# Optimization experiments

Measured on AMD Instinct MI355X. Metric: run time of the kernel, lower is better.

## Reference

```python
import jax, jax.numpy as jnp
import numpy as np
import math

B, S, D = 1024, 64, 512
H, DQ, DK = 8, 64, 64
SCALE = 1.0 / math.sqrt(D)


def setup_inputs() -> dict:
    key = jax.random.key(0)
    k1, k2, k3, k4 = jax.random.split(key, 4)
    query = jax.random.normal(k1, (B, S, D), dtype=jnp.float32)
    context = jax.random.normal(k2, (B, S, D), dtype=jnp.float32)
    # nn.Linear(input_dim, n_head*dq) weights (stored as [out, in] in torch; use [in, out] here)
    Wq = jax.random.normal(k3, (D, H * DQ), dtype=jnp.float32) * (1.0 / math.sqrt(D))
    bq = jnp.zeros((H * DQ,), dtype=jnp.float32)
    Wc = jax.random.normal(k4, (D, H * DK), dtype=jnp.float32) * (1.0 / math.sqrt(D))
    bc = jnp.zeros((H * DK,), dtype=jnp.float32)
    return {"query": query, "context": context, "Wq": Wq, "bq": bq, "Wc": Wc, "bc": bc}


def reference(query, context, Wq, bq, Wc, bc):
    bs, seq_len, _ = query.shape
    # projections -> [B, H, S, d]
    q = (query @ Wq + bq).reshape(bs, seq_len, H, DQ).transpose(0, 2, 1, 3)
    c = (context @ Wc + bc).reshape(bs, seq_len, H, DK).transpose(0, 2, 1, 3)
    # shared score matrix [B, H, Sq, Sk]
    attn = jnp.einsum('bhqd,bhkd->bhqk', q, c) * SCALE
    # direction 1: softmax over keys; NOTE: as written in the torch source,
    # the second bmm operand is the TRANSPOSED c_proj [*, d_k, S], so the
    # contraction pairs attn's key axis with c's FEATURE axis (requires S==d_k).
    c_attn = jax.nn.softmax(attn, axis=-1)
    c_coattn = jnp.einsum('bhqk,bhjk->bhqj', c_attn, c)  # [B,H,S,S(=d_k)]
    # direction 2: softmax over queries, transpose, standard weighted sum of q
    q_attn = jax.nn.softmax(attn, axis=2)
    q_coattn = jnp.einsum('bhqk,bhqd->bhkd', q_attn, q)  # [B,H,S,d_q]
    # [B, H, S, d] -> [B, S, H*d]
    c_out = c_coattn.transpose(0, 2, 1, 3).reshape(bs, seq_len, H * DK)
    q_out = q_coattn.transpose(0, 2, 1, 3).reshape(bs, seq_len, H * DQ)
    return (c_out, q_out)
```

## Files before the change

kernel.cpp:

```cpp
#include <hip/hip_runtime.h>
#include <hip/hip_bf16.h>

typedef float  f32x4 __attribute__((ext_vector_type(4)));
typedef short  s16x8 __attribute__((ext_vector_type(8)));

#define NB   1024
#define SEQ  64
#define DIM  512
#define NH   8
#define SCALE 0.044194173824159216f

static __device__ __forceinline__ unsigned short f2bf(float f) {
    unsigned u = __builtin_bit_cast(unsigned, f);
    return (unsigned short)((u + 0x8000u) >> 16);
}

static __device__ __forceinline__ f32x4 mma(s16x8 a, s16x8 b, f32x4 c) {
    return __builtin_amdgcn_mfma_f32_16x16x32_bf16(a, b, c, 0, 0, 0);
}

static __device__ __forceinline__ s16x8 cvt2(float4 a, float4 b) {
    s16x8 x;
    x[0] = (short)f2bf(a.x); x[1] = (short)f2bf(a.y);
    x[2] = (short)f2bf(a.z); x[3] = (short)f2bf(a.w);
    x[4] = (short)f2bf(b.x); x[5] = (short)f2bf(b.y);
    x[6] = (short)f2bf(b.z); x[7] = (short)f2bf(b.w);
    return x;
}

__global__ __launch_bounds__(256) void prep_weights(
    const float* __restrict__ Wq, const float* __restrict__ Wc,
    unsigned short* __restrict__ wf)
{
    int gid  = blockIdx.x * 256 + threadIdx.x;
    int m    = gid >> 15;
    int tile = (gid >> 10) & 31;
    int ks   = (gid >> 6) & 15;
    int lane = gid & 63;
    const float* W = m ? Wc : Wq;
    int col = tile * 16 + (lane & 15);
    int k0  = ks * 32 + (lane >> 4) * 8;
    unsigned short* dst = wf + (size_t)gid * 8;
#pragma unroll
    for (int j = 0; j < 8; ++j)
        dst[j] = f2bf(W[(size_t)(k0 + j) * DIM + col]);
}

__global__ __launch_bounds__(512) void fused_b(
    const float* __restrict__ query,
    const float* __restrict__ context,
    const float* __restrict__ bq,
    const float* __restrict__ bc,
    const unsigned short* __restrict__ wf,
    float* __restrict__ out)
{
    __shared__ unsigned short smem[69632];
    unsigned short* Q = smem;
    unsigned short* C = smem + 32768;

    const int tid  = threadIdx.x;
    const int lane = tid & 63;
    const int wv   = tid >> 6;
    const int l15  = lane & 15;
    const int l4   = lane >> 4;
    const int b    = blockIdx.x;

    const float* gq = query   + (size_t)b * SEQ * DIM;
    const float* gc = context + (size_t)b * SEQ * DIM;

    {
        const int row = tid >> 3;
        const int cw  = tid & 7;
        const int wsb = (cw >> 2) * 256 + (cw & 3) * 64 + row;
        const float* sq = gq + (size_t)row * DIM + cw * 8;
        const float* sc = gc + (size_t)row * DIM + cw * 8;
        float4 lq[16], lc[16];
#pragma unroll
        for (int p = 0; p < 8; ++p) {
            lq[2 * p]     = *(const float4*)(sq + p * 64);
            lq[2 * p + 1] = *(const float4*)(sq + p * 64 + 4);
        }
#pragma unroll
        for (int p = 0; p < 8; ++p) {
            lc[2 * p]     = *(const float4*)(sc + p * 64);
            lc[2 * p + 1] = *(const float4*)(sc + p * 64 + 4);
        }
#pragma unroll
        for (int p = 0; p < 8; ++p) {
            *(s16x8*)&Q[((p * 512 + wsb) ^ cw) * 8] = cvt2(lq[2 * p], lq[2 * p + 1]);
            *(s16x8*)&C[((p * 512 + wsb) ^ cw) * 8] = cvt2(lc[2 * p], lc[2 * p + 1]);
        }
    }
    __syncthreads();

    const f32x4 fz = {0.f, 0.f, 0.f, 0.f};
    f32x4 acc[4][4];

#pragma unroll
    for (int x = 0; x < 4; ++x)
#pragma unroll
        for (int y = 0; y < 4; ++y) acc[x][y] = fz;

    {
        const unsigned short* wfm = wf + 262144;
#pragma unroll
        for (int ks = 0; ks < 16; ++ks) {
            const int p  = ks >> 1;
            const int kk = ks & 1;
            s16x8 af[4], bf[4];
#pragma unroll
            for (int mt = 0; mt < 4; ++mt) {
                const int s = p * 512 + kk * 256 + l4 * 64 + mt * 16 + l15;
                af[mt] = *(const s16x8*)&C[(s ^ (4 * kk + l4)) * 8];
            }
#pragma unroll
            for (int nt = 0; nt < 4; ++nt)
                bf[nt] = *(const s16x8*)(wfm +
                         ((size_t)((wv * 4 + nt) * 16 + ks) * 64 + lane) * 8);
#pragma unroll
            for (int mt = 0; mt < 4; ++mt)
#pragma unroll
                for (int nt = 0; nt < 4; ++nt)
                    acc[mt][nt] = mma(af[mt], bf[nt], acc[mt][nt]);
        }
    }
    __syncthreads();

    unsigned short (*T)[72] = (unsigned short(*)[72])(C + wv * 4608);

#pragma unroll
    for (int nt = 0; nt < 4; ++nt) {
        float bcv = bc[wv * 64 + nt * 16 + l15];
#pragma unroll
        for (int mt = 0; mt < 4; ++mt)
#pragma unroll
            for (int r = 0; r < 4; ++r)
                T[mt * 16 + l4 * 4 + r][nt * 16 + l15] = f2bf(acc[mt][nt][r] + bcv);
    }
    s16x8 cb[4][2];
#pragma unroll
    for (int nt = 0; nt < 4; ++nt)
#pragma unroll
        for (int ks = 0; ks < 2; ++ks)
            cb[nt][ks] = *(const s16x8*)&T[nt * 16 + l15][ks * 32 + l4 * 8];

#pragma unroll
    for (int x = 0; x < 4; ++x)
#pragma unroll
        for (int y = 0; y < 4; ++y) acc[x][y] = fz;

    {
#pragma unroll
        for (int ks = 0; ks < 16; ++ks) {
            const int p  = ks >> 1;
            const int kk = ks & 1;
            s16x8 af[4], bf[4];
#pragma unroll
            for (int mt = 0; mt < 4; ++mt) {
                const int s = p * 512 + kk * 256 + l4 * 64 + mt * 16 + l15;
                af[mt] = *(const s16x8*)&Q[(s ^ (4 * kk + l4)) * 8];
            }
#pragma unroll
            for (int nt = 0; nt < 4; ++nt)
                bf[nt] = *(const s16x8*)(wf +
                         ((size_t)((wv * 4 + nt) * 16 + ks) * 64 + lane) * 8);
#pragma unroll
            for (int mt = 0; mt < 4; ++mt)
#pragma unroll
                for (int nt = 0; nt < 4; ++nt)
                    acc[mt][nt] = mma(af[mt], bf[nt], acc[mt][nt]);
        }
    }

#pragma unroll
    for (int nt = 0; nt < 4; ++nt) {
        float bqv = bq[wv * 64 + nt * 16 + l15];
#pragma unroll
        for (int mt = 0; mt < 4; ++mt)
#pragma unroll
            for (int r = 0; r < 4; ++r)
                T[mt * 16 + l4 * 4 + r][nt * 16 + l15] = f2bf(acc[mt][nt][r] + bqv);
    }
    s16x8 qa[4][2], qb[4][2];
#pragma unroll
    for (int mt = 0; mt < 4; ++mt)
#pragma unroll
        for (int ks = 0; ks < 2; ++ks)
            qa[mt][ks] = *(const s16x8*)&T[mt * 16 + l15][ks * 32 + l4 * 8];
#pragma unroll
    for (int nt = 0; nt < 4; ++nt)
#pragma unroll
        for (int ks = 0; ks < 2; ++ks) {
            s16x8 v;
#pragma unroll
            for (int j = 0; j < 8; ++j)
                v[j] = (short)T[ks * 32 + l4 * 8 + j][nt * 16 + l15];
            qb[nt][ks] = v;
        }

    f32x4 Sc[4][4];
#pragma unroll
    for (int x = 0; x < 4; ++x)
#pragma unroll
        for (int y = 0; y < 4; ++y) Sc[x][y] = fz;
#pragma unroll
    for (int ks = 0; ks < 2; ++ks)
#pragma unroll
        for (int mt = 0; mt < 4; ++mt)
#pragma unroll
            for (int nt = 0; nt < 4; ++nt)
                Sc[mt][nt] = mma(qa[mt][ks], cb[nt][ks], Sc[mt][nt]);

#pragma unroll
    for (int mt = 0; mt < 4; ++mt)
#pragma unroll
        for (int r = 0; r < 4; ++r) {
            float m = fmaxf(fmaxf(Sc[mt][0][r], Sc[mt][1][r]),
                            fmaxf(Sc[mt][2][r], Sc[mt][3][r]));
            m = fmaxf(m, __shfl_xor(m, 1));
            m = fmaxf(m, __shfl_xor(m, 2));
            m = fmaxf(m, __shfl_xor(m, 4));
            m = fmaxf(m, __shfl_xor(m, 8));
            float e[4], s = 0.f;
#pragma unroll
            for (int nt = 0; nt < 4; ++nt) { e[nt] = __expf(SCALE * (Sc[mt][nt][r] - m)); s += e[nt]; }
            s += __shfl_xor(s, 1);
            s += __shfl_xor(s, 2);
            s += __shfl_xor(s, 4);
            s += __shfl_xor(s, 8);
            float inv = 1.f / s;
            int row = mt * 16 + l4 * 4 + r;
#pragma unroll
            for (int nt = 0; nt < 4; ++nt)
                T[row][nt * 16 + l15] = f2bf(e[nt] * inv);
        }

    s16x8 pa[4][2];
#pragma unroll
    for (int mt = 0; mt < 4; ++mt)
#pragma unroll
        for (int ks = 0; ks < 2; ++ks)
            pa[mt][ks] = *(const s16x8*)&T[mt * 16 + l15][ks * 32 + l4 * 8];

#pragma unroll
    for (int nt = 0; nt < 4; ++nt) {
        float m = -1e30f;
#pragma unroll
        for (int mt = 0; mt < 4; ++mt)
#pragma unroll
            for (int r = 0; r < 4; ++r) m = fmaxf(m, Sc[mt][nt][r]);
        m = fmaxf(m, __shfl_xor(m, 16));
        m = fmaxf(m, __shfl_xor(m, 32));
        float ee[4][4], s = 0.f;
#pragma unroll
        for (int mt = 0; mt < 4; ++mt)
#pragma unroll
            for (int r = 0; r < 4; ++r) { ee[mt][r] = __expf(SCALE * (Sc[mt][nt][r] - m)); s += ee[mt][r]; }
        s += __shfl_xor(s, 16);
        s += __shfl_xor(s, 32);
        float inv = 1.f / s;
        int krow = nt * 16 + l15;
#pragma unroll
        for (int mt = 0; mt < 4; ++mt)
#pragma unroll
            for (int r = 0; r < 4; ++r)
                T[krow][mt * 16 + l4 * 4 + r] = f2bf(ee[mt][r] * inv);
    }

    f32x4 O[4][4];
#pragma unroll
    for (int x = 0; x < 4; ++x)
#pragma unroll
        for (int y = 0; y < 4; ++y) O[x][y] = fz;
#pragma unroll
    for (int ks = 0; ks < 2; ++ks)
#pragma unroll
        for (int mt = 0; mt < 4; ++mt)
#pragma unroll
            for (int nt = 0; nt < 4; ++nt)
                O[mt][nt] = mma(pa[mt][ks], cb[nt][ks], O[mt][nt]);

    float* cO = out;
#pragma unroll
    for (int mt = 0; mt < 4; ++mt)
#pragma unroll
        for (int nt = 0; nt < 4; ++nt)
#pragma unroll
            for (int r = 0; r < 4; ++r) {
                int qrow = mt * 16 + l4 * 4 + r;
                cO[((size_t)b * SEQ + qrow) * (NH * 64) + wv * 64 + nt * 16 + l15] = O[mt][nt][r];
            }

    s16x8 p2a[4][2];
#pragma unroll
    for (int mt = 0; mt < 4; ++mt)
#pragma unroll
        for (int ks = 0; ks < 2; ++ks)
            p2a[mt][ks] = *(const s16x8*)&T[mt * 16 + l15][ks * 32 + l4 * 8];

#pragma unroll
    for (int x = 0; x < 4; ++x)
#pragma unroll
        for (int y = 0; y < 4; ++y) O[x][y] = fz;
#pragma unroll
    for (int ks = 0; ks < 2; ++ks)
#pragma unroll
        for (int mt = 0; mt < 4; ++mt)
#pragma unroll
            for (int nt = 0; nt < 4; ++nt)
                O[mt][nt] = mma(p2a[mt][ks], qb[nt][ks], O[mt][nt]);

    float* qO = out + (size_t)NB * SEQ * NH * 64;
#pragma unroll
    for (int mt = 0; mt < 4; ++mt)
#pragma unroll
        for (int nt = 0; nt < 4; ++nt)
#pragma unroll
            for (int r = 0; r < 4; ++r) {
                int krow = mt * 16 + l4 * 4 + r;
                qO[((size_t)b * SEQ + krow) * (NH * 64) + wv * 64 + nt * 16 + l15] = O[mt][nt][r];
            }
}

extern "C" void kernel_launch(void* const* d_in, const int* in_sizes, int n_in,
                              void* d_out, int out_size, void* d_ws, size_t ws_size,
                              hipStream_t stream) {
    const float* query   = (const float*)d_in[0];
    const float* context = (const float*)d_in[1];
    const float* Wq      = (const float*)d_in[2];
    const float* bq      = (const float*)d_in[3];
    const float* Wc      = (const float*)d_in[4];
    const float* bc      = (const float*)d_in[5];
    float* out = (float*)d_out;

    unsigned short* wfrag = (unsigned short*)d_ws;

    prep_weights<<<256, 256, 0, stream>>>(Wq, Wc, wfrag);
    fused_b<<<NB, 512, 0, stream>>>(query, context, bq, bc, wfrag, out);
}
```

Measured before the change: 181.6 us.

## Pre-swizzle activations to bf16 and stream tiles via global_load_lds in persistent kernel

```diff
diff --git a/kernel.cpp b/kernel.cpp
--- a/kernel.cpp
+++ b/kernel.cpp
@@ -46,6 +46,288 @@
         dst[j] = f2bf(W[(size_t)(k0 + j) * DIM + col]);
 }
 
+__global__ __launch_bounds__(256) void prep_acts_swz(
+    const float* __restrict__ qin, const float* __restrict__ cin,
+    unsigned short* __restrict__ acts)
+{
+    size_t g0 = ((size_t)blockIdx.x * 256 + threadIdx.x) * 2;
+#pragma unroll
+    for (int t = 0; t < 2; ++t) {
+        size_t g  = g0 + t;
+        int    d  = (int)(g & 4095);
+        size_t tb = g >> 12;
+        const float* act = (tb >= NB)
+            ? cin + (tb - NB) * (size_t)SEQ * DIM
+            : qin + tb * (size_t)SEQ * DIM;
+        int p  = d >> 9, kk = (d >> 8) & 1, qq = (d >> 6) & 3;
+        int row = (d & 63) ^ (4 * kk + qq);
+        const float* src = act + (size_t)row * DIM + p * 64 + kk * 32 + qq * 8;
+        float4 a  = *(const float4*)src;
+        float4 b2 = *(const float4*)(src + 4);
+        *(s16x8*)(acts + g * 8) = cvt2(a, b2);
+    }
+}
+
+#define GLL16(GP, LP)                                                          \
+    __builtin_amdgcn_global_load_lds(                                          \
+        (const unsigned int __attribute__((address_space(1)))*)(const void*)(GP), \
+        (unsigned int __attribute__((address_space(3)))*)(void*)(LP), 16, 0, 0)
+
+__global__ __launch_bounds__(512) void fused_gll(
+    const unsigned short* __restrict__ acts,
+    const float* __restrict__ bq,
+    const float* __restrict__ bc,
+    const unsigned short* __restrict__ wf,
+    float* __restrict__ out)
+{
+    __shared__ unsigned short smem[69632];
+    unsigned short* Q = smem;
+    unsigned short* C = smem + 32768;
+
+    const int tid  = threadIdx.x;
+    const int lane = tid & 63;
+    const int wv   = tid >> 6;
+    const int l15  = lane & 15;
+    const int l4   = lane >> 4;
+    const int blk  = blockIdx.x;
+
+    unsigned short (*T)[72] = (unsigned short(*)[72])(C + wv * 4608);
+    const f32x4 fz = {0.f, 0.f, 0.f, 0.f};
+
+#define STAGE_TILE(SRC, REGION)                                                \
+    {                                                                          \
+        _Pragma("unroll")                                                      \
+        for (int i_ = 0; i_ < 8; ++i_) {                                       \
+            const int so_ = wv * 4096 + i_ * 512;                              \
+            GLL16((SRC) + so_ + lane * 8, &(REGION)[so_]);                     \
+        }                                                                      \
+    }
+
+#define GEMM16(REGION, WFM)                                                    \
+    {                                                                          \
+        _Pragma("unroll")                                                      \
+        for (int ks = 0; ks < 16; ++ks) {                                      \
+            const int p_ = ks >> 1, kk_ = ks & 1;                              \
+            s16x8 af[4], bf[4];                                                \
+            _Pragma("unroll")                                                  \
+            for (int mt = 0; mt < 4; ++mt) {                                   \
+                const int s_ = p_ * 512 + kk_ * 256 + l4 * 64 + mt * 16 + l15; \
+                af[mt] = *(const s16x8*)&(REGION)[(s_ ^ (4 * kk_ + l4)) * 8];  \
+            }                                                                  \
+            _Pragma("unroll")                                                  \
+            for (int nt = 0; nt < 4; ++nt)                                     \
+                bf[nt] = *(const s16x8*)((WFM) +                               \
+                         ((size_t)((wv * 4 + nt) * 16 + ks) * 64 + lane) * 8); \
+            _Pragma("unroll")                                                  \
+            for (int mt = 0; mt < 4; ++mt)                                     \
+                _Pragma("unroll")                                              \
+                for (int nt = 0; nt < 4; ++nt)                                 \
+                    acc[mt][nt] = mma(af[mt], bf[nt], acc[mt][nt]);            \
+        }                                                                      \
+    }
+
+    STAGE_TILE(acts + (size_t)blk * 32768, Q);
+    STAGE_TILE(acts + (size_t)(NB + blk) * 32768, C);
+    __syncthreads();
+
+    for (int n = 0; n < 4; ++n) {
+        const int b = blk + 256 * n;
+
+        f32x4 acc[4][4];
+#pragma unroll
+        for (int x = 0; x < 4; ++x)
+#pragma unroll
+            for (int y = 0; y < 4; ++y) acc[x][y] = fz;
+
+        GEMM16(C, wf + 262144);
+        __syncthreads();
+
+#pragma unroll
+        for (int nt = 0; nt < 4; ++nt) {
+            float bcv = bc[wv * 64 + nt * 16 + l15];
+#pragma unroll
+            for (int mt = 0; mt < 4; ++mt)
+#pragma unroll
+                for (int r = 0; r < 4; ++r)
+                    T[mt * 16 + l4 * 4 + r][nt * 16 + l15] = f2bf(acc[mt][nt][r] + bcv);
+        }
+        s16x8 cb[4][2];
+#pragma unroll
+        for (int nt = 0; nt < 4; ++nt)
+#pragma unroll
+            for (int ks = 0; ks < 2; ++ks)
+                cb[nt][ks] = *(const s16x8*)&T[nt * 16 + l15][ks * 32 + l4 * 8];
+
+#pragma unroll
+        for (int x = 0; x < 4; ++x)
+#pragma unroll
+            for (int y = 0; y < 4; ++y) acc[x][y] = fz;
+        GEMM16(Q, wf);
+        __syncthreads();
+
+        if (n < 3) STAGE_TILE(acts + (size_t)(b + 256) * 32768, Q);
+
+#pragma unroll
+        for (int nt = 0; nt < 4; ++nt) {
+            float bqv = bq[wv * 64 + nt * 16 + l15];
+#pragma unroll
+            for (int mt = 0; mt < 4; ++mt)
+#pragma unroll
+                for (int r = 0; r < 4; ++r)
+                    T[mt * 16 + l4 * 4 + r][nt * 16 + l15] = f2bf(acc[mt][nt][r] + bqv);
+        }
+        s16x8 qa[4][2], qb[4][2];
+#pragma unroll
+        for (int mt = 0; mt < 4; ++mt)
+#pragma unroll
+            for (int ks = 0; ks < 2; ++ks)
+                qa[mt][ks] = *(const s16x8*)&T[mt * 16 + l15][ks * 32 + l4 * 8];
+#pragma unroll
+        for (int nt = 0; nt < 4; ++nt)
+#pragma unroll
+            for (int ks = 0; ks < 2; ++ks) {
+                s16x8 v;
+#pragma unroll
+                for (int j = 0; j < 8; ++j)
+                    v[j] = (short)T[ks * 32 + l4 * 8 + j][nt * 16 + l15];
+                qb[nt][ks] = v;
+            }
+
+        f32x4 Sc[4][4];
+#pragma unroll
+        for (int x = 0; x < 4; ++x)
+#pragma unroll
+            for (int y = 0; y < 4; ++y) Sc[x][y] = fz;
+#pragma unroll
+        for (int ks = 0; ks < 2; ++ks)
+#pragma unroll
+            for (int mt = 0; mt < 4; ++mt)
+#pragma unroll
+                for (int nt = 0; nt < 4; ++nt)
+                    Sc[mt][nt] = mma(qa[mt][ks], cb[nt][ks], Sc[mt][nt]);
+
+#pragma unroll
+        for (int mt = 0; mt < 4; ++mt)
+#pragma unroll
+            for (int r = 0; r < 4; ++r) {
+                float m = fmaxf(fmaxf(Sc[mt][0][r], Sc[mt][1][r]),
+                                fmaxf(Sc[mt][2][r], Sc[mt][3][r]));
+                m = fmaxf(m, __shfl_xor(m, 1));
+                m = fmaxf(m, __shfl_xor(m, 2));
+                m = fmaxf(m, __shfl_xor(m, 4));
+                m = fmaxf(m, __shfl_xor(m, 8));
+                float e[4], s = 0.f;
+#pragma unroll
+                for (int nt = 0; nt < 4; ++nt) { e[nt] = __expf(SCALE * (Sc[mt][nt][r] - m)); s += e[nt]; }
+                s += __shfl_xor(s, 1);
+                s += __shfl_xor(s, 2);
+                s += __shfl_xor(s, 4);
+                s += __shfl_xor(s, 8);
+                float inv = 1.f / s;
+                int r3 = mt * 16 + l4 * 4 + r;
+#pragma unroll
+                for (int nt = 0; nt < 4; ++nt)
+                    T[r3][nt * 16 + l15] = f2bf(e[nt] * inv);
+            }
+
+        s16x8 pa[4][2];
+#pragma unroll
+        for (int mt = 0; mt < 4; ++mt)
+#pragma unroll
+            for (int ks = 0; ks < 2; ++ks)
+                pa[mt][ks] = *(const s16x8*)&T[mt * 16 + l15][ks * 32 + l4 * 8];
+
+#pragma unroll
+        for (int nt = 0; nt < 4; ++nt) {
+            float m = -1e30f;
+#pragma unroll
+            for (int mt = 0; mt < 4; ++mt)
+#pragma unroll
+                for (int r = 0; r < 4; ++r) m = fmaxf(m, Sc[mt][nt][r]);
+            m = fmaxf(m, __shfl_xor(m, 16));
+            m = fmaxf(m, __shfl_xor(m, 32));
+            float ee[4][4], s = 0.f;
+#pragma unroll
+            for (int mt = 0; mt < 4; ++mt)
+#pragma unroll
+                for (int r = 0; r < 4; ++r) { ee[mt][r] = __expf(SCALE * (Sc[mt][nt][r] - m)); s += ee[mt][r]; }
+            s += __shfl_xor(s, 16);
+            s += __shfl_xor(s, 32);
+            float inv = 1.f / s;
+            int krow = nt * 16 + l15;
+#pragma unroll
+            for (int mt = 0; mt < 4; ++mt)
+#pragma unroll
+                for (int r = 0; r < 4; ++r)
+                    T[krow][mt * 16 + l4 * 4 + r] = f2bf(ee[mt][r] * inv);
+        }
+
+        f32x4 O[4][4];
+#pragma unroll
+        for (int x = 0; x < 4; ++x)
+#pragma unroll
+            for (int y = 0; y < 4; ++y) O[x][y] = fz;
+#pragma unroll
+        for (int ks = 0; ks < 2; ++ks)
+#pragma unroll
+            for (int mt = 0; mt < 4; ++mt)
+#pragma unroll
+                for (int nt = 0; nt < 4; ++nt)
+                    O[mt][nt] = mma(pa[mt][ks], cb[nt][ks], O[mt][nt]);
+
+        float* cO = out;
+#pragma unroll
+        for (int mt = 0; mt < 4; ++mt)
+#pragma unroll
+            for (int nt = 0; nt < 4; ++nt)
+#pragma unroll
+                for (int r = 0; r < 4; ++r) {
+                    int qrow = mt * 16 + l4 * 4 + r;
+                    cO[((size_t)b * SEQ + qrow) * (NH * 64) + wv * 64 + nt * 16 + l15] = O[mt][nt][r];
+                }
+
+        s16x8 p2a[4][2];
+#pragma unroll
+        for (int mt = 0; mt < 4; ++mt)
+#pragma unroll
+            for (int ks = 0; ks < 2; ++ks)
+                p2a[mt][ks] = *(const s16x8*)&T[mt * 16 + l15][ks * 32 + l4 * 8];
+
+#pragma unroll
+        for (int x = 0; x < 4; ++x)
+#pragma unroll
+            for (int y = 0; y < 4; ++y) O[x][y] = fz;
+#pragma unroll
+        for (int ks = 0; ks < 2; ++ks)
+#pragma unroll
+            for (int mt = 0; mt < 4; ++mt)
+#pragma unroll
+                for (int nt = 0; nt < 4; ++nt)
+                    O[mt][nt] = mma(p2a[mt][ks], qb[nt][ks], O[mt][nt]);
+
+        float* qO = out + (size_t)NB * SEQ * NH * 64;
+#pragma unroll
+        for (int mt = 0; mt < 4; ++mt)
+#pragma unroll
+            for (int nt = 0; nt < 4; ++nt)
+#pragma unroll
+                for (int r = 0; r < 4; ++r) {
+                    int krow = mt * 16 + l4 * 4 + r;
+                    qO[((size_t)b * SEQ + krow) * (NH * 64) + wv * 64 + nt * 16 + l15] = O[mt][nt][r];
+                }
+
+        __syncthreads();
+
+        if (n < 3) {
+            STAGE_TILE(acts + (size_t)(NB + b + 256) * 32768, C);
+            __syncthreads();
+        }
+    }
+
+#undef STAGE_TILE
+#undef GEMM16
+}
+
 __global__ __launch_bounds__(512) void fused_b(
     const float* __restrict__ query,
     const float* __restrict__ context,
@@ -95,7 +377,6 @@
 
     const f32x4 fz = {0.f, 0.f, 0.f, 0.f};
     f32x4 acc[4][4];
-
 #pragma unroll
     for (int x = 0; x < 4; ++x)
 #pragma unroll
@@ -334,7 +615,14 @@
     float* out = (float*)d_out;
 
     unsigned short* wfrag = (unsigned short*)d_ws;
+    unsigned short* acts  = wfrag + 524288;
+    const size_t need = (524288 + (size_t)2 * NB * 4096 * 8) * sizeof(unsigned short);
 
     prep_weights<<<256, 256, 0, stream>>>(Wq, Wc, wfrag);
-    fused_b<<<NB, 512, 0, stream>>>(query, context, bq, bc, wfrag, out);
-}
+    if (ws_size >= need) {
+        prep_acts_swz<<<16384, 256, 0, stream>>>(query, context, acts);
+        fused_gll<<<256, 512, 0, stream>>>(acts, bq, bc, wfrag, out);
+    } else {
+        fused_b<<<NB, 512, 0, stream>>>(query, context, bq, bc, wfrag, out);
+    }
+}
```

Measured after the change: 598.3 us. 3.29x slower.
